# Optimization experiments

Hardware: AMD Instinct MI355X
Metric: run time of the kernel (lower is better)

Reference implementation:

```python
import jax, jax.numpy as jnp
import numpy as np

MEM_DIM = 128
ORDER = 256
THETA = 256.0
BATCH = 16
SEQ = 256
IN_DIM = 128


def _lmu_discrete_AB(order, theta):
    # Legendre delay network matrices (same construction as GenerateABMatrix)
    Q = np.arange(order, dtype=np.float64)
    R = (2.0 * Q + 1.0)[:, None]
    j, i = np.meshgrid(Q, Q)
    A = np.where(i < j, -1.0, (-1.0) ** (i - j + 1)) * R          # (O, O)
    B = ((-1.0) ** Q[:, None]) * R                                 # (O, 1)
    At = A.T / theta                                               # transposed system
    Bt = B.T / theta                                               # (1, O)
    # ZOH discretization on the transposed system: expm of padded block matrix
    em = np.concatenate([np.concatenate([At, Bt], axis=0),
                         np.zeros((order + 1, 1))], axis=1)        # (O+1, O+1)
    ms = jax.scipy.linalg.expm(jnp.asarray(em, jnp.float32))
    Ad = ms[:order, :order]                                        # (O, O)
    Bd = ms[order:, :order]                                        # (1, O)
    return Ad, Bd


def setup_inputs() -> dict:
    key = jax.random.key(0)
    kx, kw = jax.random.split(key)
    x = jax.random.normal(kx, (BATCH, SEQ, IN_DIM), dtype=jnp.float32)
    # glorot-uniform MemoryKernel (inputDim, MemoryDim)
    limit = np.sqrt(6.0 / (IN_DIM + MEM_DIM))
    memory_kernel = jax.random.uniform(kw, (IN_DIM, MEM_DIM), dtype=jnp.float32,
                                       minval=-limit, maxval=limit)
    A, B_mat = _lmu_discrete_AB(ORDER, THETA)
    return {"x": x, "memory_kernel": memory_kernel, "A": A, "B_mat": B_mat}


def reference(x, memory_kernel, A, B_mat):
    """LRMUCell (hiddenCell=None, no memory/hidden feedback) unrolled over SEQ.

    Per step: u_t = x_t @ K ; m_t = m_{t-1} @ Ad + u_t[:, :, None] * Bd
    Returns the final flattened memory state (batch, MemoryDim * Order).
    """
    Bsz, T, D = x.shape
    M = memory_kernel.shape[1]
    O = A.shape[0]
    # No feedback into u, so the input projection can be hoisted out of the scan.
    u_all = jnp.einsum('btd,dm->tbm', x, memory_kernel)  # (T, B, M)

    def step(m, u):
        # m: (B, M, O); u: (B, M)
        # (B,M,1) @ (1,O) is an outer product along the last axes
        m_new = jnp.matmul(m, A) + u[..., None] * B_mat
        return m_new, None

    m0 = jnp.zeros((Bsz, M, O), dtype=x.dtype)
    m_final, _ = jax.lax.scan(step, m0, u_all)
    return m_final.reshape(Bsz, M * O)
```

## Files before the change

kernel.cpp:

```cpp
#include <hip/hip_runtime.h>


#define SEQ_T 256
#define DIM 128
#define ORD 256
#define BMROWS 2048

#define OFF_U 0
#define OFF_P (OFF_U + SEQ_T * BMROWS)
#define APSTRIDE (ORD * ORD + 2048)
#define OFF_AP (OFF_P + ORD * ORD + 2048)
#define OFF_FLAGS (OFF_AP + 7 * APSTRIDE + 2048)

#define LD_A(p) \
  __hip_atomic_load((p), __ATOMIC_RELAXED, __HIP_MEMORY_SCOPE_AGENT)
#define ST_A(p, v) \
  __hip_atomic_store((p), (v), __ATOMIC_RELAXED, __HIP_MEMORY_SCOPE_AGENT)

__device__ __forceinline__ void gbar(unsigned* flags, unsigned* gen,
                                     unsigned target) {
  asm volatile("s_waitcnt vmcnt(0)" ::: "memory");
  __syncthreads();
  const int tid = threadIdx.x;
  if (blockIdx.x == 0) {
    if (tid == 0) ST_A(&flags[0], target);
    while (LD_A(&flags[tid]) < target) __builtin_amdgcn_s_sleep(1);
    __syncthreads();
    if (tid == 0) ST_A(gen, target);
  } else {
    if (tid == 0) {
      ST_A(&flags[blockIdx.x], target);
      while (LD_A(gen) < target) __builtin_amdgcn_s_sleep(1);
    }
  }
  __syncthreads();
}

__global__ __launch_bounds__(256) void lrmu_all(
    const float* __restrict__ x, const float* __restrict__ K,
    const float* __restrict__ A, const float* __restrict__ Bm,
    float* __restrict__ out, float* __restrict__ ws) {
  __shared__ __align__(16) float Slds[ORD * 64];
  __shared__ __align__(16) float lsb[2048];
  __shared__ __align__(16) float redb[4 * 320];
  float* U = ws + OFF_U;
  float* P = ws + OFF_P;
  unsigned* flags = (unsigned*)(ws + OFF_FLAGS);
  unsigned* gen = flags + 320;
  const int blk = blockIdx.x, tid = threadIdx.x;

  {
    int b = blk >> 4, tc = blk & 15;
    float* xs = Slds;
    for (int idx = tid; idx < 16 * DIM; idx += 256)
      xs[idx] = x[(b * SEQ_T + tc * 16) * DIM + idx];
    __syncthreads();
    int m = tid & 127, th = tid >> 7;
    float acc[8] = {};
#pragma unroll 8
    for (int d = 0; d < DIM; ++d) {
      float kv = K[d * DIM + m];
#pragma unroll
      for (int r = 0; r < 8; ++r)
        acc[r] = fmaf(xs[(th * 8 + r) * DIM + d], kv, acc[r]);
    }
#pragma unroll
    for (int r = 0; r < 8; ++r)
      ST_A(&U[(tc * 16 + th * 8 + r) * BMROWS + b * DIM + m], acc[r]);
    if (blk == 0) ST_A(&P[tid], Bm[tid]);
    __syncthreads();
  }

  const int rg = blk >> 2, cg = blk & 3;
  const int lane = tid & 63, q = tid >> 6;
  const int ir = lane >> 4, c4 = (lane & 15) * 4;
  for (int k = 0; k < 8; ++k) {
    const float* S = (k == 0) ? A : (ws + OFF_AP + (k - 1) * APSTRIDE);
    float* Snew = ws + OFF_AP + ((k < 7) ? k : 6) * APSTRIDE;
    const int half = 1 << k;
    const int nsq = (k < 7) ? 4 : 0;
    const int ndb = (k == 7) ? 2 : (rg < half ? 1 : 0);
    const int nrows = nsq + ndb;

#pragma unroll
    for (int s = 0; s < 5; ++s) {
      float v = 0.f;
      if (s < nsq) {
        v = S[(4 * rg + s) * ORD + tid];
      } else if (s - nsq < ndb) {
        int d = rg + 64 * (s - nsq);
        v = (k == 0) ? Bm[tid] : P[d * ORD + tid];
      }
      lsb[s * ORD + tid] = v;
    }
#pragma unroll
    for (int j = 0; j < 16; ++j) {
      int f = tid + 256 * j;
      int i = f >> 4, cc = (f & 15) * 4;
      *(float4*)&Slds[i * 64 + cc] =
          *(const float4*)&S[i * ORD + cg * 64 + cc];
    }
    __syncthreads();

    float acc[5][4] = {};
#pragma unroll 4
    for (int ii = 0; ii < 16; ++ii) {
      int i = q * 64 + 4 * ii + ir;
      float4 sv = *(const float4*)&Slds[i * 64 + c4];
#pragma unroll
      for (int s = 0; s < 5; ++s) {
        float lv = lsb[s * ORD + i];
        acc[s][0] = fmaf(lv, sv.x, acc[s][0]);
        acc[s][1] = fmaf(lv, sv.y, acc[s][1]);
        acc[s][2] = fmaf(lv, sv.z, acc[s][2]);
        acc[s][3] = fmaf(lv, sv.w, acc[s][3]);
      }
    }
#pragma unroll
    for (int s = 0; s < 5; ++s)
#pragma unroll
      for (int w = 0; w < 4; ++w) {
        acc[s][w] += __shfl_xor(acc[s][w], 16);
        acc[s][w] += __shfl_xor(acc[s][w], 32);
      }
    if (ir == 0) {
#pragma unroll
      for (int s = 0; s < 5; ++s)
        *(float4*)&redb[q * 320 + s * 64 + c4] =
            make_float4(acc[s][0], acc[s][1], acc[s][2], acc[s][3]);
    }
    __syncthreads();
    for (int o = tid; o < 320; o += 256) {
      int s = o >> 6, c = o & 63;
      if (s < nrows) {
        float sum = redb[o] + redb[320 + o] + redb[640 + o] + redb[960 + o];
        if (s < nsq) {
          ST_A(&Snew[(4 * rg + s) * ORD + cg * 64 + c], sum);
        } else {
          int d = rg + 64 * (s - nsq);
          ST_A(&P[(half + d) * ORD + cg * 64 + c], sum);
        }
      }
    }
    gbar(flags, gen, (unsigned)(k + 1));
  }

  {
    float* us = lsb;
    float* redo = Slds;
    int bm0 = blk * 8;
    for (int idx = tid; idx < SEQ_T * 8; idx += 256) {
      int t = idx >> 3, r = idx & 7;
      us[idx] = U[t * BMROWS + bm0 + r];
    }
    __syncthreads();
    int c4o = lane * 4, qo = q;
    float ao[8][4] = {};
#pragma unroll 4
    for (int tt = 0; tt < 64; ++tt) {
      int t = qo * 64 + tt;
      float4 pv = *(const float4*)&P[(SEQ_T - 1 - t) * ORD + c4o];
      float4 u0 = *(const float4*)&us[t * 8];
      float4 u1 = *(const float4*)&us[t * 8 + 4];
      float uv[8] = {u0.x, u0.y, u0.z, u0.w, u1.x, u1.y, u1.z, u1.w};
      float pw[4] = {pv.x, pv.y, pv.z, pv.w};
#pragma unroll
      for (int r = 0; r < 8; ++r)
#pragma unroll
        for (int w = 0; w < 4; ++w)
          ao[r][w] = fmaf(uv[r], pw[w], ao[r][w]);
    }
#pragma unroll
    for (int r = 0; r < 8; ++r)
      *(float4*)&redo[qo * 2048 + r * 256 + c4o] =
          make_float4(ao[r][0], ao[r][1], ao[r][2], ao[r][3]);
    __syncthreads();
#pragma unroll
    for (int j = 0; j < 8; ++j) {
      int o = tid + 256 * j;
      float s = redo[o] + redo[2048 + o] + redo[4096 + o] + redo[6144 + o];
      out[bm0 * ORD + o] = s;
    }
  }
}

extern "C" void kernel_launch(void* const* d_in, const int* in_sizes, int n_in,
                              void* d_out, int out_size, void* d_ws,
                              size_t ws_size, hipStream_t stream) {
  const float* x = (const float*)d_in[0];
  const float* K = (const float*)d_in[1];
  const float* A = (const float*)d_in[2];
  const float* Bm = (const float*)d_in[3];
  float* out = (float*)d_out;
  float* ws = (float*)d_ws;

  hipMemsetAsync(ws + OFF_FLAGS, 0, 2048, stream);
  lrmu_all<<<256, 256, 0, stream>>>(x, K, A, Bm, out, ws);
}
```

Measured before the change: 118.0 us.

## Drop final doubling stage and apply A^128 to the early-half contribution

The last squaring/doubling stage, which built P rows 128..255, is removed, together with its global barrier. The output is instead split into two halves: the late half uses P rows 0..127 directly, and the early half's partial sum is multiplied by the precomputed A^128 matrix in each block. The grid barrier also changes: block 0 now releases the other blocks through 8 spread generation flags instead of one, and the sleep durations change. This removes one grid-wide sync and one matrix stage, at the cost of a per-block 256x256 matvec over 8 rows.

```diff
diff --git a/kernel.cpp b/kernel.cpp
--- a/kernel.cpp
+++ b/kernel.cpp
@@ -17,20 +17,20 @@
 #define ST_A(p, v) \
   __hip_atomic_store((p), (v), __ATOMIC_RELAXED, __HIP_MEMORY_SCOPE_AGENT)
 
-__device__ __forceinline__ void gbar(unsigned* flags, unsigned* gen,
-                                     unsigned target) {
+__device__ __forceinline__ void gbar(unsigned* flags, unsigned target) {
   asm volatile("s_waitcnt vmcnt(0)" ::: "memory");
   __syncthreads();
   const int tid = threadIdx.x;
   if (blockIdx.x == 0) {
     if (tid == 0) ST_A(&flags[0], target);
-    while (LD_A(&flags[tid]) < target) __builtin_amdgcn_s_sleep(1);
-    __syncthreads();
-    if (tid == 0) ST_A(gen, target);
+    while (LD_A(&flags[tid]) < target) __builtin_amdgcn_s_sleep(2);
+    __syncthreads();
+    if (tid < 8) ST_A(&flags[256 + tid * 16], target);
   } else {
     if (tid == 0) {
       ST_A(&flags[blockIdx.x], target);
-      while (LD_A(gen) < target) __builtin_amdgcn_s_sleep(1);
+      unsigned* g = &flags[256 + (blockIdx.x & 7) * 16];
+      while (LD_A(g) < target) __builtin_amdgcn_s_sleep(3);
     }
   }
   __syncthreads();
@@ -46,7 +46,6 @@
   float* U = ws + OFF_U;
   float* P = ws + OFF_P;
   unsigned* flags = (unsigned*)(ws + OFF_FLAGS);
-  unsigned* gen = flags + 320;
   const int blk = blockIdx.x, tid = threadIdx.x;
 
   {
@@ -74,22 +73,20 @@
   const int rg = blk >> 2, cg = blk & 3;
   const int lane = tid & 63, q = tid >> 6;
   const int ir = lane >> 4, c4 = (lane & 15) * 4;
-  for (int k = 0; k < 8; ++k) {
+  for (int k = 0; k < 7; ++k) {
     const float* S = (k == 0) ? A : (ws + OFF_AP + (k - 1) * APSTRIDE);
-    float* Snew = ws + OFF_AP + ((k < 7) ? k : 6) * APSTRIDE;
+    float* Snew = ws + OFF_AP + k * APSTRIDE;
     const int half = 1 << k;
-    const int nsq = (k < 7) ? 4 : 0;
-    const int ndb = (k == 7) ? 2 : (rg < half ? 1 : 0);
-    const int nrows = nsq + ndb;
+    const int ndb = (rg < half) ? 1 : 0;
+    const int nrows = 4 + ndb;
 
 #pragma unroll
     for (int s = 0; s < 5; ++s) {
       float v = 0.f;
-      if (s < nsq) {
+      if (s < 4) {
         v = S[(4 * rg + s) * ORD + tid];
-      } else if (s - nsq < ndb) {
-        int d = rg + 64 * (s - nsq);
-        v = (k == 0) ? Bm[tid] : P[d * ORD + tid];
+      } else if (ndb) {
+        v = (k == 0) ? Bm[tid] : P[rg * ORD + tid];
       }
       lsb[s * ORD + tid] = v;
     }
@@ -134,18 +131,18 @@
       int s = o >> 6, c = o & 63;
       if (s < nrows) {
         float sum = redb[o] + redb[320 + o] + redb[640 + o] + redb[960 + o];
-        if (s < nsq) {
+        if (s < 4) {
           ST_A(&Snew[(4 * rg + s) * ORD + cg * 64 + c], sum);
         } else {
-          int d = rg + 64 * (s - nsq);
-          ST_A(&P[(half + d) * ORD + cg * 64 + c], sum);
+          ST_A(&P[(half + rg) * ORD + cg * 64 + c], sum);
         }
       }
     }
-    gbar(flags, gen, (unsigned)(k + 1));
+    gbar(flags, (unsigned)(k + 1));
   }
 
   {
+    const float* S128 = ws + OFF_AP + 6 * APSTRIDE;
     float* us = lsb;
     float* redo = Slds;
     int bm0 = blk * 8;
@@ -154,33 +151,77 @@
       us[idx] = U[t * BMROWS + bm0 + r];
     }
     __syncthreads();
-    int c4o = lane * 4, qo = q;
-    float ao[8][4] = {};
-#pragma unroll 4
-    for (int tt = 0; tt < 64; ++tt) {
-      int t = qo * 64 + tt;
-      float4 pv = *(const float4*)&P[(SEQ_T - 1 - t) * ORD + c4o];
-      float4 u0 = *(const float4*)&us[t * 8];
-      float4 u1 = *(const float4*)&us[t * 8 + 4];
+    int c4o = lane * 4;
+    float acc[8][4];
+#pragma unroll
+    for (int r = 0; r < 8; ++r)
+#pragma unroll
+      for (int w = 0; w < 4; ++w) acc[r][w] = 0.f;
+#pragma unroll 4
+    for (int jj = 0; jj < 32; ++jj) {
+      int j = q * 32 + jj;
+      float4 pv = *(const float4*)&P[j * ORD + c4o];
+      float4 u0 = *(const float4*)&us[(255 - j) * 8];
+      float4 u1 = *(const float4*)&us[(255 - j) * 8 + 4];
       float uv[8] = {u0.x, u0.y, u0.z, u0.w, u1.x, u1.y, u1.z, u1.w};
       float pw[4] = {pv.x, pv.y, pv.z, pv.w};
 #pragma unroll
       for (int r = 0; r < 8; ++r)
 #pragma unroll
         for (int w = 0; w < 4; ++w)
-          ao[r][w] = fmaf(uv[r], pw[w], ao[r][w]);
-    }
-#pragma unroll
-    for (int r = 0; r < 8; ++r)
-      *(float4*)&redo[qo * 2048 + r * 256 + c4o] =
-          make_float4(ao[r][0], ao[r][1], ao[r][2], ao[r][3]);
-    __syncthreads();
-#pragma unroll
-    for (int j = 0; j < 8; ++j) {
-      int o = tid + 256 * j;
-      float s = redo[o] + redo[2048 + o] + redo[4096 + o] + redo[6144 + o];
-      out[bm0 * ORD + o] = s;
-    }
+          acc[r][w] = fmaf(uv[r], pw[w], acc[r][w]);
+    }
+#pragma unroll
+    for (int r = 0; r < 8; ++r)
+      *(float4*)&redo[q * 4096 + r * 256 + c4o] =
+          make_float4(acc[r][0], acc[r][1], acc[r][2], acc[r][3]);
+#pragma unroll
+    for (int r = 0; r < 8; ++r)
+#pragma unroll
+      for (int w = 0; w < 4; ++w) acc[r][w] = 0.f;
+#pragma unroll 4
+    for (int jj = 0; jj < 32; ++jj) {
+      int j = q * 32 + jj;
+      float4 pv = *(const float4*)&P[j * ORD + c4o];
+      float4 u0 = *(const float4*)&us[(127 - j) * 8];
+      float4 u1 = *(const float4*)&us[(127 - j) * 8 + 4];
+      float uv[8] = {u0.x, u0.y, u0.z, u0.w, u1.x, u1.y, u1.z, u1.w};
+      float pw[4] = {pv.x, pv.y, pv.z, pv.w};
+#pragma unroll
+      for (int r = 0; r < 8; ++r)
+#pragma unroll
+        for (int w = 0; w < 4; ++w)
+          acc[r][w] = fmaf(uv[r], pw[w], acc[r][w]);
+    }
+#pragma unroll
+    for (int r = 0; r < 8; ++r)
+      *(float4*)&redo[q * 4096 + (8 + r) * 256 + c4o] =
+          make_float4(acc[r][0], acc[r][1], acc[r][2], acc[r][3]);
+    __syncthreads();
+
+    int c = tid;
+    float hreg[8];
+#pragma unroll
+    for (int r = 0; r < 8; ++r)
+      hreg[r] = redo[r * 256 + c] + redo[4096 + r * 256 + c] +
+                redo[8192 + r * 256 + c] + redo[12288 + r * 256 + c];
+    __syncthreads();
+#pragma unroll
+    for (int r = 0; r < 8; ++r)
+      lsb[r * 256 + c] = redo[(8 + r) * 256 + c] + redo[4096 + (8 + r) * 256 + c] +
+                         redo[8192 + (8 + r) * 256 + c] +
+                         redo[12288 + (8 + r) * 256 + c];
+    __syncthreads();
+
+#pragma unroll 4
+    for (int i = 0; i < 256; ++i) {
+      float sv = S128[i * ORD + c];
+#pragma unroll
+      for (int r = 0; r < 8; ++r)
+        hreg[r] = fmaf(lsb[r * 256 + i], sv, hreg[r]);
+    }
+#pragma unroll
+    for (int r = 0; r < 8; ++r) out[(bm0 + r) * ORD + c] = hreg[r];
   }
 }
 
```

Result: slower. 130.6 us (+10.7%).

## Split grid barrier and overlap output accumulation with power-doubling steps

Applied to the files above, without the earlier changes.

The last doubling stage, which computed P rows 128..255, is dropped. The output is split into a direct sum over the first 128 powers plus a correction term g·A^128 that reuses the stored A^128 matrix. The grid barrier is split into arrive and wait phases, and each block accumulates its share of the output from newly available P rows between them, hiding barrier latency behind useful work. In exchange there is an extra 256x256 matrix-vector stage at the end and the output contraction order changes, which affects rounding.

```diff
diff --git a/kernel.cpp b/kernel.cpp
--- a/kernel.cpp
+++ b/kernel.cpp
@@ -17,20 +17,20 @@
 #define ST_A(p, v) \
   __hip_atomic_store((p), (v), __ATOMIC_RELAXED, __HIP_MEMORY_SCOPE_AGENT)
 
-__device__ __forceinline__ void gbar(unsigned* flags, unsigned* gen,
-                                     unsigned target) {
+__device__ __forceinline__ void gbar_arrive(unsigned* flags, unsigned target) {
   asm volatile("s_waitcnt vmcnt(0)" ::: "memory");
   __syncthreads();
+  if (threadIdx.x == 0) ST_A(&flags[blockIdx.x], target);
+}
+__device__ __forceinline__ void gbar_wait(unsigned* flags, unsigned target) {
   const int tid = threadIdx.x;
   if (blockIdx.x == 0) {
-    if (tid == 0) ST_A(&flags[0], target);
     while (LD_A(&flags[tid]) < target) __builtin_amdgcn_s_sleep(1);
     __syncthreads();
-    if (tid == 0) ST_A(gen, target);
+    if (tid == 0) ST_A(&flags[320], target);
   } else {
     if (tid == 0) {
-      ST_A(&flags[blockIdx.x], target);
-      while (LD_A(gen) < target) __builtin_amdgcn_s_sleep(1);
+      while (LD_A(&flags[320]) < target) __builtin_amdgcn_s_sleep(1);
     }
   }
   __syncthreads();
@@ -41,13 +41,15 @@
     const float* __restrict__ A, const float* __restrict__ Bm,
     float* __restrict__ out, float* __restrict__ ws) {
   __shared__ __align__(16) float Slds[ORD * 64];
-  __shared__ __align__(16) float lsb[2048];
+  __shared__ __align__(16) float lsb[5 * ORD];
   __shared__ __align__(16) float redb[4 * 320];
+  __shared__ __align__(16) float us[SEQ_T * 8];
   float* U = ws + OFF_U;
   float* P = ws + OFF_P;
   unsigned* flags = (unsigned*)(ws + OFF_FLAGS);
-  unsigned* gen = flags + 320;
   const int blk = blockIdx.x, tid = threadIdx.x;
+  const int bm0 = blk * 8;
+  float hAcc[8] = {}, gAcc[8] = {};
 
   {
     int b = blk >> 4, tc = blk & 15;
@@ -74,22 +76,20 @@
   const int rg = blk >> 2, cg = blk & 3;
   const int lane = tid & 63, q = tid >> 6;
   const int ir = lane >> 4, c4 = (lane & 15) * 4;
-  for (int k = 0; k < 8; ++k) {
+  for (int k = 0; k < 7; ++k) {
     const float* S = (k == 0) ? A : (ws + OFF_AP + (k - 1) * APSTRIDE);
-    float* Snew = ws + OFF_AP + ((k < 7) ? k : 6) * APSTRIDE;
+    float* Snew = ws + OFF_AP + k * APSTRIDE;
     const int half = 1 << k;
-    const int nsq = (k < 7) ? 4 : 0;
-    const int ndb = (k == 7) ? 2 : (rg < half ? 1 : 0);
-    const int nrows = nsq + ndb;
+    const int ndb = (rg < half) ? 1 : 0;
+    const int nrows = 4 + ndb;
 
 #pragma unroll
     for (int s = 0; s < 5; ++s) {
       float v = 0.f;
-      if (s < nsq) {
+      if (s < 4) {
         v = S[(4 * rg + s) * ORD + tid];
-      } else if (s - nsq < ndb) {
-        int d = rg + 64 * (s - nsq);
-        v = (k == 0) ? Bm[tid] : P[d * ORD + tid];
+      } else if (ndb) {
+        v = (k == 0) ? Bm[tid] : P[rg * ORD + tid];
       }
       lsb[s * ORD + tid] = v;
     }
@@ -134,52 +134,98 @@
       int s = o >> 6, c = o & 63;
       if (s < nrows) {
         float sum = redb[o] + redb[320 + o] + redb[640 + o] + redb[960 + o];
-        if (s < nsq) {
+        if (s < 4) {
           ST_A(&Snew[(4 * rg + s) * ORD + cg * 64 + c], sum);
         } else {
-          int d = rg + 64 * (s - nsq);
-          ST_A(&P[(half + d) * ORD + cg * 64 + c], sum);
+          ST_A(&P[(half + rg) * ORD + cg * 64 + c], sum);
         }
       }
     }
-    gbar(flags, gen, (unsigned)(k + 1));
+    gbar_arrive(flags, (unsigned)(k + 1));
+
+    if (k >= 1) {
+      if (k == 1) {
+        for (int idx = tid; idx < SEQ_T * 8; idx += 256) {
+          int t = idx >> 3, r = idx & 7;
+          us[idx] = U[t * BMROWS + bm0 + r];
+        }
+        __syncthreads();
+      }
+      int jlo = (k == 1) ? 0 : (1 << (k - 1));
+      int jhi = 1 << k;
+      for (int j = jlo; j < jhi; ++j) {
+        float pv = P[j * ORD + tid];
+        const float4 h0 = *(const float4*)&us[(255 - j) * 8];
+        const float4 h1 = *(const float4*)&us[(255 - j) * 8 + 4];
+        const float4 g0 = *(const float4*)&us[(127 - j) * 8];
+        const float4 g1 = *(const float4*)&us[(127 - j) * 8 + 4];
+        hAcc[0] = fmaf(h0.x, pv, hAcc[0]); hAcc[1] = fmaf(h0.y, pv, hAcc[1]);
+        hAcc[2] = fmaf(h0.z, pv, hAcc[2]); hAcc[3] = fmaf(h0.w, pv, hAcc[3]);
+        hAcc[4] = fmaf(h1.x, pv, hAcc[4]); hAcc[5] = fmaf(h1.y, pv, hAcc[5]);
+        hAcc[6] = fmaf(h1.z, pv, hAcc[6]); hAcc[7] = fmaf(h1.w, pv, hAcc[7]);
+        gAcc[0] = fmaf(g0.x, pv, gAcc[0]); gAcc[1] = fmaf(g0.y, pv, gAcc[1]);
+        gAcc[2] = fmaf(g0.z, pv, gAcc[2]); gAcc[3] = fmaf(g0.w, pv, gAcc[3]);
+        gAcc[4] = fmaf(g1.x, pv, gAcc[4]); gAcc[5] = fmaf(g1.y, pv, gAcc[5]);
+        gAcc[6] = fmaf(g1.z, pv, gAcc[6]); gAcc[7] = fmaf(g1.w, pv, gAcc[7]);
+      }
+    }
+    gbar_wait(flags, (unsigned)(k + 1));
   }
 
   {
-    float* us = lsb;
-    float* redo = Slds;
-    int bm0 = blk * 8;
-    for (int idx = tid; idx < SEQ_T * 8; idx += 256) {
-      int t = idx >> 3, r = idx & 7;
-      us[idx] = U[t * BMROWS + bm0 + r];
-    }
-    __syncthreads();
-    int c4o = lane * 4, qo = q;
-    float ao[8][4] = {};
+    for (int j = 64; j < 128; ++j) {
+      float pv = P[j * ORD + tid];
+      const float4 h0 = *(const float4*)&us[(255 - j) * 8];
+      const float4 h1 = *(const float4*)&us[(255 - j) * 8 + 4];
+      const float4 g0 = *(const float4*)&us[(127 - j) * 8];
+      const float4 g1 = *(const float4*)&us[(127 - j) * 8 + 4];
+      hAcc[0] = fmaf(h0.x, pv, hAcc[0]); hAcc[1] = fmaf(h0.y, pv, hAcc[1]);
+      hAcc[2] = fmaf(h0.z, pv, hAcc[2]); hAcc[3] = fmaf(h0.w, pv, hAcc[3]);
+      hAcc[4] = fmaf(h1.x, pv, hAcc[4]); hAcc[5] = fmaf(h1.y, pv, hAcc[5]);
+      hAcc[6] = fmaf(h1.z, pv, hAcc[6]); hAcc[7] = fmaf(h1.w, pv, hAcc[7]);
+      gAcc[0] = fmaf(g0.x, pv, gAcc[0]); gAcc[1] = fmaf(g0.y, pv, gAcc[1]);
+      gAcc[2] = fmaf(g0.z, pv, gAcc[2]); gAcc[3] = fmaf(g0.w, pv, gAcc[3]);
+      gAcc[4] = fmaf(g1.x, pv, gAcc[4]); gAcc[5] = fmaf(g1.y, pv, gAcc[5]);
+      gAcc[6] = fmaf(g1.z, pv, gAcc[6]); gAcc[7] = fmaf(g1.w, pv, gAcc[7]);
+    }
+    __syncthreads();
+
+    float* Gt = Slds;
+    float* redo = Slds + 4096;
+#pragma unroll
+    for (int r = 0; r < 8; ++r) Gt[tid * 12 + r] = gAcc[r];
+    __syncthreads();
+
+    const float* S128 = ws + OFF_AP + 6 * APSTRIDE;
+    int team = tid >> 6, tc4 = (tid & 63) * 4;
+    float hloc[8][4] = {};
 #pragma unroll 4
-    for (int tt = 0; tt < 64; ++tt) {
-      int t = qo * 64 + tt;
-      float4 pv = *(const float4*)&P[(SEQ_T - 1 - t) * ORD + c4o];
-      float4 u0 = *(const float4*)&us[t * 8];
-      float4 u1 = *(const float4*)&us[t * 8 + 4];
-      float uv[8] = {u0.x, u0.y, u0.z, u0.w, u1.x, u1.y, u1.z, u1.w};
-      float pw[4] = {pv.x, pv.y, pv.z, pv.w};
-#pragma unroll
-      for (int r = 0; r < 8; ++r)
-#pragma unroll
-        for (int w = 0; w < 4; ++w)
-          ao[r][w] = fmaf(uv[r], pw[w], ao[r][w]);
+    for (int ii = 0; ii < 64; ++ii) {
+      int i = team * 64 + ii;
+      float4 sv = *(const float4*)&S128[i * ORD + tc4];
+      float4 ga = *(const float4*)&Gt[i * 12];
+      float4 gb = *(const float4*)&Gt[i * 12 + 4];
+      float gv[8] = {ga.x, ga.y, ga.z, ga.w, gb.x, gb.y, gb.z, gb.w};
+#pragma unroll
+      for (int r = 0; r < 8; ++r) {
+        hloc[r][0] = fmaf(gv[r], sv.x, hloc[r][0]);
+        hloc[r][1] = fmaf(gv[r], sv.y, hloc[r][1]);
+        hloc[r][2] = fmaf(gv[r], sv.z, hloc[r][2]);
+        hloc[r][3] = fmaf(gv[r], sv.w, hloc[r][3]);
+      }
     }
 #pragma unroll
     for (int r = 0; r < 8; ++r)
-      *(float4*)&redo[qo * 2048 + r * 256 + c4o] =
-          make_float4(ao[r][0], ao[r][1], ao[r][2], ao[r][3]);
-    __syncthreads();
-#pragma unroll
-    for (int j = 0; j < 8; ++j) {
-      int o = tid + 256 * j;
-      float s = redo[o] + redo[2048 + o] + redo[4096 + o] + redo[6144 + o];
-      out[bm0 * ORD + o] = s;
+      *(float4*)&redo[team * 2048 + r * 256 + tc4] =
+          make_float4(hloc[r][0], hloc[r][1], hloc[r][2], hloc[r][3]);
+    __syncthreads();
+
+    int c = tid;
+#pragma unroll
+    for (int r = 0; r < 8; ++r) {
+      float gbv = redo[r * 256 + c] + redo[2048 + r * 256 + c] +
+                  redo[4096 + r * 256 + c] + redo[6144 + r * 256 + c];
+      out[(bm0 + r) * ORD + c] = hAcc[r] + gbv;
     }
   }
 }
```

New measurement: 123.7 us. 4.9% more time.

## Stop doubling at 64 powers and combine chunks via Horner with A^64

Applied to the files above, without the earlier changes.

The power-doubling phase now stops after six steps, computing A^64 and the first 64 rows of P, so the last two grid-wide barriers and the full 256x256 matmul rounds are removed. In the final phase each wave computes a partial sum over one 64-step chunk, and the four partials are combined with three Horner steps that each multiply by A^64, reading A^64 from global memory. This trades two global barriers and their squaring work for extra per-block matmuls in the epilogue, plus extra LDS for the chunk buffers.

```diff
diff --git a/kernel.cpp b/kernel.cpp
--- a/kernel.cpp
+++ b/kernel.cpp
@@ -17,8 +17,7 @@
 #define ST_A(p, v) \
   __hip_atomic_store((p), (v), __ATOMIC_RELAXED, __HIP_MEMORY_SCOPE_AGENT)
 
-__device__ __forceinline__ void gbar(unsigned* flags, unsigned* gen,
-                                     unsigned target) {
+__device__ __forceinline__ void gbar(unsigned* flags, unsigned target) {
   asm volatile("s_waitcnt vmcnt(0)" ::: "memory");
   __syncthreads();
   const int tid = threadIdx.x;
@@ -26,11 +25,11 @@
     if (tid == 0) ST_A(&flags[0], target);
     while (LD_A(&flags[tid]) < target) __builtin_amdgcn_s_sleep(1);
     __syncthreads();
-    if (tid == 0) ST_A(gen, target);
+    if (tid == 0) ST_A(&flags[320], target);
   } else {
     if (tid == 0) {
       ST_A(&flags[blockIdx.x], target);
-      while (LD_A(gen) < target) __builtin_amdgcn_s_sleep(1);
+      while (LD_A(&flags[320]) < target) __builtin_amdgcn_s_sleep(1);
     }
   }
   __syncthreads();
@@ -41,12 +40,12 @@
     const float* __restrict__ A, const float* __restrict__ Bm,
     float* __restrict__ out, float* __restrict__ ws) {
   __shared__ __align__(16) float Slds[ORD * 64];
-  __shared__ __align__(16) float lsb[2048];
+  __shared__ __align__(16) float lsb[5 * ORD];
   __shared__ __align__(16) float redb[4 * 320];
+  __shared__ __align__(16) float us[SEQ_T * 8];
   float* U = ws + OFF_U;
   float* P = ws + OFF_P;
   unsigned* flags = (unsigned*)(ws + OFF_FLAGS);
-  unsigned* gen = flags + 320;
   const int blk = blockIdx.x, tid = threadIdx.x;
 
   {
@@ -74,22 +73,20 @@
   const int rg = blk >> 2, cg = blk & 3;
   const int lane = tid & 63, q = tid >> 6;
   const int ir = lane >> 4, c4 = (lane & 15) * 4;
-  for (int k = 0; k < 8; ++k) {
+  for (int k = 0; k < 6; ++k) {
     const float* S = (k == 0) ? A : (ws + OFF_AP + (k - 1) * APSTRIDE);
-    float* Snew = ws + OFF_AP + ((k < 7) ? k : 6) * APSTRIDE;
+    float* Snew = ws + OFF_AP + k * APSTRIDE;
     const int half = 1 << k;
-    const int nsq = (k < 7) ? 4 : 0;
-    const int ndb = (k == 7) ? 2 : (rg < half ? 1 : 0);
-    const int nrows = nsq + ndb;
+    const int ndb = (rg < half) ? 1 : 0;
+    const int nrows = 4 + ndb;
 
 #pragma unroll
     for (int s = 0; s < 5; ++s) {
       float v = 0.f;
-      if (s < nsq) {
+      if (s < 4) {
         v = S[(4 * rg + s) * ORD + tid];
-      } else if (s - nsq < ndb) {
-        int d = rg + 64 * (s - nsq);
-        v = (k == 0) ? Bm[tid] : P[d * ORD + tid];
+      } else if (ndb) {
+        v = (k == 0) ? Bm[tid] : P[rg * ORD + tid];
       }
       lsb[s * ORD + tid] = v;
     }
@@ -134,32 +131,34 @@
       int s = o >> 6, c = o & 63;
       if (s < nrows) {
         float sum = redb[o] + redb[320 + o] + redb[640 + o] + redb[960 + o];
-        if (s < nsq) {
+        if (s < 4) {
           ST_A(&Snew[(4 * rg + s) * ORD + cg * 64 + c], sum);
         } else {
-          int d = rg + 64 * (s - nsq);
-          ST_A(&P[(half + d) * ORD + cg * 64 + c], sum);
+          ST_A(&P[(half + rg) * ORD + cg * 64 + c], sum);
         }
       }
     }
-    gbar(flags, gen, (unsigned)(k + 1));
+    gbar(flags, (unsigned)(k + 1));
   }
 
   {
-    float* us = lsb;
-    float* redo = Slds;
-    int bm0 = blk * 8;
+    float* Garr = Slds;
+    float* redo = Slds + 8192;
+    const float* A64 = ws + OFF_AP + 5 * APSTRIDE;
+    const int bm0 = blk * 8;
+    const int c4o = lane * 4;
+
     for (int idx = tid; idx < SEQ_T * 8; idx += 256) {
       int t = idx >> 3, r = idx & 7;
       us[idx] = U[t * BMROWS + bm0 + r];
     }
     __syncthreads();
-    int c4o = lane * 4, qo = q;
-    float ao[8][4] = {};
+
+    float acc[8][4] = {};
 #pragma unroll 4
-    for (int tt = 0; tt < 64; ++tt) {
-      int t = qo * 64 + tt;
-      float4 pv = *(const float4*)&P[(SEQ_T - 1 - t) * ORD + c4o];
+    for (int j = 0; j < 64; ++j) {
+      float4 pv = *(const float4*)&P[j * ORD + c4o];
+      int t = 255 - 64 * q - j;
       float4 u0 = *(const float4*)&us[t * 8];
       float4 u1 = *(const float4*)&us[t * 8 + 4];
       float uv[8] = {u0.x, u0.y, u0.z, u0.w, u1.x, u1.y, u1.z, u1.w};
@@ -168,18 +167,49 @@
       for (int r = 0; r < 8; ++r)
 #pragma unroll
         for (int w = 0; w < 4; ++w)
-          ao[r][w] = fmaf(uv[r], pw[w], ao[r][w]);
+          acc[r][w] = fmaf(uv[r], pw[w], acc[r][w]);
     }
 #pragma unroll
     for (int r = 0; r < 8; ++r)
-      *(float4*)&redo[qo * 2048 + r * 256 + c4o] =
-          make_float4(ao[r][0], ao[r][1], ao[r][2], ao[r][3]);
-    __syncthreads();
-#pragma unroll
-    for (int j = 0; j < 8; ++j) {
-      int o = tid + 256 * j;
-      float s = redo[o] + redo[2048 + o] + redo[4096 + o] + redo[6144 + o];
-      out[bm0 * ORD + o] = s;
+      *(float4*)&Garr[q * 2048 + r * 256 + c4o] =
+          make_float4(acc[r][0], acc[r][1], acc[r][2], acc[r][3]);
+    __syncthreads();
+
+    for (int s = 2; s >= 0; --s) {
+      const float* T = &Garr[(s + 1) * 2048];
+      float hl[8][4] = {};
+#pragma unroll 4
+      for (int ii = 0; ii < 64; ++ii) {
+        int i = q * 64 + ii;
+        float4 av = *(const float4*)&A64[i * ORD + c4o];
+        float tv[8];
+#pragma unroll
+        for (int r = 0; r < 8; ++r) tv[r] = T[r * 256 + i];
+#pragma unroll
+        for (int r = 0; r < 8; ++r) {
+          hl[r][0] = fmaf(tv[r], av.x, hl[r][0]);
+          hl[r][1] = fmaf(tv[r], av.y, hl[r][1]);
+          hl[r][2] = fmaf(tv[r], av.z, hl[r][2]);
+          hl[r][3] = fmaf(tv[r], av.w, hl[r][3]);
+        }
+      }
+#pragma unroll
+      for (int r = 0; r < 8; ++r)
+        *(float4*)&redo[q * 2048 + r * 256 + c4o] =
+            make_float4(hl[r][0], hl[r][1], hl[r][2], hl[r][3]);
+      __syncthreads();
+      const int c = tid;
+#pragma unroll
+      for (int r = 0; r < 8; ++r) {
+        float v = redo[r * 256 + c] + redo[2048 + r * 256 + c] +
+                  redo[4096 + r * 256 + c] + redo[6144 + r * 256 + c] +
+                  Garr[s * 2048 + r * 256 + c];
+        if (s > 0)
+          Garr[s * 2048 + r * 256 + c] = v;
+        else
+          out[(bm0 + r) * ORD + c] = v;
+      }
+      __syncthreads();
     }
   }
 }
```

Result: slower. 125.8 us (+6.7%).
